# Optimization experiments

Hardware: AMD Instinct MI355X
Metric: run time of the kernel (lower is better)

Reference implementation:

```python
import jax, jax.numpy as jnp
import numpy as np

N_NODES = 100000
N_EDGES = 1600000
IN_FEATS = 128
OUT_FEATS = 128
LN_EPS = 1e-5


def setup_inputs() -> dict:
    key = jax.random.key(0)
    k_h, k_w, k_b, k_src, k_dst = jax.random.split(key, 5)
    stdv = 1.0 / np.sqrt(OUT_FEATS)
    return {
        "h": jax.random.normal(k_h, (N_NODES, IN_FEATS), dtype=jnp.float32),
        "weight": jax.random.uniform(k_w, (IN_FEATS, OUT_FEATS), dtype=jnp.float32, minval=-stdv, maxval=stdv),
        "bias": jax.random.uniform(k_b, (OUT_FEATS,), dtype=jnp.float32, minval=-stdv, maxval=stdv),
        "gamma": jnp.ones((OUT_FEATS,), dtype=jnp.float32),
        "beta": jnp.zeros((OUT_FEATS,), dtype=jnp.float32),
        "src": jax.random.randint(k_src, (N_EDGES,), 0, N_NODES, dtype=jnp.int32),
        "dst": jax.random.randint(k_dst, (N_EDGES,), 0, N_NODES, dtype=jnp.int32),
    }


def reference(h, weight, bias, gamma, beta, src, dst):
    n = h.shape[0]
    # in-degree norm: 1/deg with inf -> 0 (isolated nodes)
    deg = jax.ops.segment_sum(jnp.ones_like(dst, dtype=h.dtype), dst, num_segments=n)
    norm = jnp.where(deg > 0, 1.0 / deg, 0.0)[:, None]  # [N, 1]
    # update_all(copy_src, sum): scatter-add of source features onto destinations
    ah = jax.ops.segment_sum(h[src], dst, num_segments=n)  # [N, in_feats]
    x = ah * norm
    x = x @ weight + bias  # [N, out_feats]
    # LayerNorm over feature dim with affine params
    mu = jnp.mean(x, axis=-1, keepdims=True)
    var = jnp.mean(jnp.square(x - mu), axis=-1, keepdims=True)
    x = (x - mu) * jax.lax.rsqrt(var + LN_EPS) * gamma + beta
    return jax.nn.relu(x)
```

## Files before the change

### kernel.cpp

```cpp
#include <hip/hip_runtime.h>
#include <hip/hip_fp16.h>

#define F 128
#define SCANB 1024
#define NBLK 256
#define GB2 512
#define BSHIFT 7
#define MAXNB 2048
#define SMEM_BYTES 43264

typedef __attribute__((ext_vector_type(8))) short short8;
typedef __attribute__((ext_vector_type(4))) float f32x4;

static __device__ __forceinline__ short f2bf(float f) {
    union { float f; unsigned u; } v; v.f = f;
    unsigned r = v.u + 0x7FFF + ((v.u >> 16) & 1);
    return (short)(r >> 16);
}
static __device__ __forceinline__ __half2 h2(unsigned u) {
    return __builtin_bit_cast(__half2, u);
}
static __device__ __forceinline__ uint4 pack8h(float a0,float a1,float a2,float a3,
                                               float a4,float a5,float a6,float a7) {
    uint4 o;
    o.x = __builtin_bit_cast(unsigned, __floats2half2_rn(a0, a1));
    o.y = __builtin_bit_cast(unsigned, __floats2half2_rn(a2, a3));
    o.z = __builtin_bit_cast(unsigned, __floats2half2_rn(a4, a5));
    o.w = __builtin_bit_cast(unsigned, __floats2half2_rn(a6, a7));
    return o;
}

__global__ __launch_bounds__(256) void k_gemm_hist(
    const float* __restrict__ h, const float* __restrict__ w,
    unsigned* __restrict__ hb, const int* __restrict__ dst,
    int* __restrict__ mat, int* __restrict__ done,
    int n_nodes, int n_edges, int nb, int hblk) {
    __shared__ alignas(16) char smem[SMEM_BYTES];
    const int tid = threadIdx.x;
    const int bid = blockIdx.x;

    if (bid == 0 && tid == 0 && done) *done = 0;

    if (bid < hblk) {
        int* lh = (int*)smem;
        for (int i = tid; i < nb; i += 256) lh[i] = 0;
        __syncthreads();
        const int epb = (n_edges + hblk - 1) / hblk;
        const int e0 = bid * epb, e1 = min(e0 + epb, n_edges);
        for (int e = e0 + tid; e < e1; e += 256)
            atomicAdd(&lh[dst[e] >> BSHIFT], 1);
        __syncthreads();
        for (int i = tid; i < nb; i += 256)
            mat[(size_t)i * NBLK + bid] = lh[i];
        return;
    }

    short* wt = (short*)smem;
    float* xs = (float*)(smem + 34816);
    {
        int n = tid & 127;
        for (int k = tid >> 7; k < 128; k += 2)
            wt[n * 136 + k] = f2bf(w[(size_t)k * 128 + n]);
    }
    __syncthreads();

    const int wv = tid >> 6, l = tid & 63, lr = l & 15, lk = l >> 4, q = l & 15;
    const int step = (gridDim.x - hblk) * 64;
    float* xw = xs + wv * (4 * 132);

    for (int base = (bid - hblk) * 64; base < n_nodes; base += step) {
        const int row = base + wv * 16 + lr;
        const bool valid = row < n_nodes;

        short8 af[4];
        #pragma unroll
        for (int kk = 0; kk < 4; ++kk) {
            int k0 = kk * 32 + lk * 8;
            float4 a0{0,0,0,0}, a1{0,0,0,0};
            if (valid) {
                a0 = *(const float4*)(h + (size_t)row * F + k0);
                a1 = *(const float4*)(h + (size_t)row * F + k0 + 4);
            }
            af[kk] = short8{ f2bf(a0.x), f2bf(a0.y), f2bf(a0.z), f2bf(a0.w),
                             f2bf(a1.x), f2bf(a1.y), f2bf(a1.z), f2bf(a1.w) };
        }
        f32x4 acc[8];
        #pragma unroll
        for (int n = 0; n < 8; ++n) acc[n] = f32x4{0, 0, 0, 0};
        #pragma unroll
        for (int kk = 0; kk < 4; ++kk) {
            const int kb = kk * 32 + lk * 8;
            #pragma unroll
            for (int n = 0; n < 8; ++n) {
                short8 bfr = *(const short8*)(&wt[(n * 16 + lr) * 136 + kb]);
                acc[n] = __builtin_amdgcn_mfma_f32_16x16x32_bf16(af[kk], bfr, acc[n], 0, 0, 0);
            }
        }
        #pragma unroll
        for (int r = 0; r < 4; ++r) {
            #pragma unroll
            for (int n = 0; n < 8; ++n)
                xw[lk * 132 + n * 16 + lr] = acc[n][r];
            int grow = base + wv * 16 + lk * 4 + r;
            float4 a = *(const float4*)&xw[lk * 132 + q * 8];
            float4 b = *(const float4*)&xw[lk * 132 + q * 8 + 4];
            uint4 o = pack8h(a.x, a.y, a.z, a.w, b.x, b.y, b.z, b.w);
            if (grow < n_nodes)
                ((uint4*)hb)[(size_t)grow * 16 + q] = o;
        }
    }
}

__global__ __launch_bounds__(SCANB) void k_scan_ab(const int* in, int* out,
                                                   int* bsum, int* done, int n) {
    __shared__ int tmp[SCANB];
    __shared__ bool amLast;
    int i = blockIdx.x * SCANB + threadIdx.x;
    int v = (i < n) ? in[i] : 0;
    tmp[threadIdx.x] = v;
    __syncthreads();
    for (int off = 1; off < SCANB; off <<= 1) {
        int t = (threadIdx.x >= off) ? tmp[threadIdx.x - off] : 0;
        __syncthreads();
        tmp[threadIdx.x] += t;
        __syncthreads();
    }
    if (i < n) out[i] = tmp[threadIdx.x] - v;
    if (threadIdx.x == SCANB - 1) {
        bsum[blockIdx.x] = tmp[SCANB - 1];
        __threadfence();
        int old = atomicAdd(done, 1);
        amLast = (old == (int)gridDim.x - 1);
    }
    __syncthreads();
    if (amLast) {
        __threadfence();
        const int ns = gridDim.x;
        int w = (threadIdx.x < ns) ? ((volatile int*)bsum)[threadIdx.x] : 0;
        __syncthreads();
        tmp[threadIdx.x] = w;
        __syncthreads();
        for (int off = 1; off < SCANB; off <<= 1) {
            int t = (threadIdx.x >= off) ? tmp[threadIdx.x - off] : 0;
            __syncthreads();
            tmp[threadIdx.x] += t;
            __syncthreads();
        }
        if (threadIdx.x < ns) bsum[threadIdx.x] = tmp[threadIdx.x] - w;
    }
}

__global__ __launch_bounds__(SCANB) void k_scan_a(const int* in, int* out,
                                                  int* bsum, int n) {
    __shared__ int tmp[SCANB];
    int i = blockIdx.x * SCANB + threadIdx.x;
    int v = (i < n) ? in[i] : 0;
    tmp[threadIdx.x] = v;
    __syncthreads();
    for (int off = 1; off < SCANB; off <<= 1) {
        int t = (threadIdx.x >= off) ? tmp[threadIdx.x - off] : 0;
        __syncthreads();
        tmp[threadIdx.x] += t;
        __syncthreads();
    }
    if (i < n) out[i] = tmp[threadIdx.x] - v;
    if (threadIdx.x == SCANB - 1) bsum[blockIdx.x] = tmp[SCANB - 1];
}

__global__ __launch_bounds__(512) void k_scan_b(int* bsum, int nb) {
    __shared__ int tmp[512];
    int i = threadIdx.x;
    int v = (i < nb) ? bsum[i] : 0;
    tmp[i] = v;
    __syncthreads();
    for (int off = 1; off < 512; off <<= 1) {
        int t = (i >= off) ? tmp[i - off] : 0;
        __syncthreads();
        tmp[i] += t;
        __syncthreads();
    }
    if (i < nb) bsum[i] = tmp[i] - v;
}

__global__ __launch_bounds__(SCANB) void k_scan_c(int* out, const int* bsum, int n) {
    int i = blockIdx.x * SCANB + threadIdx.x;
    if (i < n) out[i] += bsum[blockIdx.x];
}

__global__ __launch_bounds__(512) void k_part_scatter(
    const int* __restrict__ src, const int* __restrict__ dst,
    const int* __restrict__ mat, const int* __restrict__ bsum,
    unsigned* __restrict__ binned, int n_edges, int nb, int epb) {
    __shared__ int lbase[MAXNB];
    const int bid = blockIdx.x;
    for (int i = threadIdx.x; i < nb; i += 512) {
        int idx = i * NBLK + bid;
        lbase[i] = mat[idx] + bsum[idx >> 10];
    }
    __syncthreads();
    int e0 = bid * epb;
    int e1 = min(e0 + epb, n_edges);
    for (int e = e0 + threadIdx.x; e < e1; e += 512) {
        int d = dst[e];
        int b = d >> BSHIFT;
        int pos = atomicAdd(&lbase[b], 1);
        binned[pos] = ((unsigned)(d & ((1 << BSHIFT) - 1)) << 25) | (unsigned)src[e];
    }
}

__global__ __launch_bounds__(512) void k_bin_to_csr(
    const unsigned* __restrict__ binned, const int* __restrict__ mat,
    const int* __restrict__ bsum, int* __restrict__ deg, int* __restrict__ offs,
    int* __restrict__ esrc, int n_edges, int n_nodes, int nb) {
    __shared__ int ldeg[128], loffs[128], lcur[128];
    int b = blockIdx.x;
    int i0 = b * NBLK;
    int start = mat[i0] + bsum[i0 >> 10];
    int end = n_edges;
    if (b + 1 < nb) {
        int i1 = (b + 1) * NBLK;
        end = mat[i1] + bsum[i1 >> 10];
    }
    int cnt = end - start;
    int base_node = b << BSHIFT;
    int nn = min(1 << BSHIFT, n_nodes - base_node);
    for (int i = threadIdx.x; i < nn; i += 512) { ldeg[i] = 0; lcur[i] = 0; }
    __syncthreads();
    for (int i = threadIdx.x; i < cnt; i += 512)
        atomicAdd(&ldeg[binned[start + i] >> 25], 1);
    __syncthreads();
    if (threadIdx.x == 0) {
        int run = 0;
        for (int i = 0; i < nn; ++i) { loffs[i] = run; run += ldeg[i]; }
    }
    __syncthreads();
    for (int i = threadIdx.x; i < nn; i += 512) {
        deg[base_node + i]  = ldeg[i];
        offs[base_node + i] = start + loffs[i];
    }
    for (int i = threadIdx.x; i < cnt; i += 512) {
        unsigned p = binned[start + i];
        int ln = p >> 25;
        int pos = start + loffs[ln] + atomicAdd(&lcur[ln], 1);
        esrc[pos] = (int)(p & ((1u << 25) - 1));
    }
}

__global__ __launch_bounds__(256) void k_hist(const int* __restrict__ dst,
                                              int* __restrict__ deg, int n_edges) {
    int e = blockIdx.x * 256 + threadIdx.x;
    if (e < n_edges) atomicAdd(&deg[dst[e]], 1);
}

__global__ __launch_bounds__(256) void k_scatter_idx(
    const int* __restrict__ src, const int* __restrict__ dst,
    const int* __restrict__ offs, int* __restrict__ cursor,
    int* __restrict__ esrc, int n_edges) {
    int e = blockIdx.x * 256 + threadIdx.x;
    if (e >= n_edges) return;
    int d = dst[e];
    int pos = offs[d] + atomicAdd(&cursor[d], 1);
    esrc[pos] = src[e];
}

__global__ __launch_bounds__(256) void k_gather_ln(
    const unsigned* __restrict__ hb, const int* __restrict__ esrc,
    const int* __restrict__ offs, const int* __restrict__ deg,
    const float* __restrict__ bias, const float* __restrict__ gamma,
    const float* __restrict__ beta, float* __restrict__ out, int n_nodes) {
    int t = blockIdx.x * 256 + threadIdx.x;
    int node = t >> 6;
    int l = t & 63;
    if (node >= n_nodes) return;
    const int g = l >> 4;
    const int q = l & 15;

    const int start = offs[node];
    const int dn = deg[node];
    const int end = start + dn;

    __half2 c0 = __floats2half2_rn(0.f, 0.f);
    __half2 c1 = c0, c2 = c0, c3 = c0;
    int i = start;
    for (; i + 16 <= end; i += 16) {
        int s0 = esrc[i + g];
        int s1 = esrc[i + 4 + g];
        int s2 = esrc[i + 8 + g];
        int s3 = esrc[i + 12 + g];
        uint4 v0 = *((const uint4*)(hb + (size_t)s0 * 64 + q * 4));
        uint4 v1 = *((const uint4*)(hb + (size_t)s1 * 64 + q * 4));
        uint4 v2 = *((const uint4*)(hb + (size_t)s2 * 64 + q * 4));
        uint4 v3 = *((const uint4*)(hb + (size_t)s3 * 64 + q * 4));
        c0 = __hadd2(c0, __hadd2(__hadd2(h2(v0.x), h2(v1.x)), __hadd2(h2(v2.x), h2(v3.x))));
        c1 = __hadd2(c1, __hadd2(__hadd2(h2(v0.y), h2(v1.y)), __hadd2(h2(v2.y), h2(v3.y))));
        c2 = __hadd2(c2, __hadd2(__hadd2(h2(v0.z), h2(v1.z)), __hadd2(h2(v2.z), h2(v3.z))));
        c3 = __hadd2(c3, __hadd2(__hadd2(h2(v0.w), h2(v1.w)), __hadd2(h2(v2.w), h2(v3.w))));
    }
    for (; i + 8 <= end; i += 8) {
        int s0 = esrc[i + g];
        int s1 = esrc[i + 4 + g];
        uint4 v0 = *((const uint4*)(hb + (size_t)s0 * 64 + q * 4));
        uint4 v1 = *((const uint4*)(hb + (size_t)s1 * 64 + q * 4));
        c0 = __hadd2(c0, __hadd2(h2(v0.x), h2(v1.x)));
        c1 = __hadd2(c1, __hadd2(h2(v0.y), h2(v1.y)));
        c2 = __hadd2(c2, __hadd2(h2(v0.z), h2(v1.z)));
        c3 = __hadd2(c3, __hadd2(h2(v0.w), h2(v1.w)));
    }
    for (; i < end; i += 4) {
        int e = i + g;
        if (e < end) {
            int s = esrc[e];
            uint4 v = *((const uint4*)(hb + (size_t)s * 64 + q * 4));
            c0 = __hadd2(c0, h2(v.x));
            c1 = __hadd2(c1, h2(v.y));
            c2 = __hadd2(c2, h2(v.z));
            c3 = __hadd2(c3, h2(v.w));
        }
    }
    float2 p0 = __half22float2(c0), p1 = __half22float2(c1);
    float2 p2 = __half22float2(c2), p3 = __half22float2(c3);
    float a0 = p0.x, a1 = p0.y, a2 = p1.x, a3 = p1.y;
    float a4 = p2.x, a5 = p2.y, a6 = p3.x, a7 = p3.y;

    #pragma unroll
    for (int m = 16; m <= 32; m <<= 1) {
        a0 += __shfl_xor(a0, m); a1 += __shfl_xor(a1, m);
        a2 += __shfl_xor(a2, m); a3 += __shfl_xor(a3, m);
        a4 += __shfl_xor(a4, m); a5 += __shfl_xor(a5, m);
        a6 += __shfl_xor(a6, m); a7 += __shfl_xor(a7, m);
    }
    float4 bs0 = *(const float4*)(bias  + q * 8);
    float4 bs1 = *(const float4*)(bias  + q * 8 + 4);
    const float nv = dn > 0 ? 1.0f / (float)dn : 0.0f;
    float f0 = a0 * nv + bs0.x, f1 = a1 * nv + bs0.y;
    float f2 = a2 * nv + bs0.z, f3 = a3 * nv + bs0.w;
    float f4 = a4 * nv + bs1.x, f5 = a5 * nv + bs1.y;
    float f6 = a6 * nv + bs1.z, f7 = a7 * nv + bs1.w;

    float s  = ((f0 + f1) + (f2 + f3)) + ((f4 + f5) + (f6 + f7));
    float q2 = ((f0*f0 + f1*f1) + (f2*f2 + f3*f3)) + ((f4*f4 + f5*f5) + (f6*f6 + f7*f7));
    #pragma unroll
    for (int m = 1; m <= 8; m <<= 1) {
        s  += __shfl_xor(s, m);
        q2 += __shfl_xor(q2, m);
    }
    float mu   = s * (1.0f / F);
    float var  = q2 * (1.0f / F) - mu * mu;
    float rstd = rsqrtf(var + 1e-5f);

    if (g == 0) {
        float4 gm0 = *(const float4*)(gamma + q * 8);
        float4 gm1 = *(const float4*)(gamma + q * 8 + 4);
        float4 bt0 = *(const float4*)(beta  + q * 8);
        float4 bt1 = *(const float4*)(beta  + q * 8 + 4);
        float4 o0, o1;
        o0.x = fmaxf((f0 - mu) * rstd * gm0.x + bt0.x, 0.0f);
        o0.y = fmaxf((f1 - mu) * rstd * gm0.y + bt0.y, 0.0f);
        o0.z = fmaxf((f2 - mu) * rstd * gm0.z + bt0.z, 0.0f);
        o0.w = fmaxf((f3 - mu) * rstd * gm0.w + bt0.w, 0.0f);
        o1.x = fmaxf((f4 - mu) * rstd * gm1.x + bt1.x, 0.0f);
        o1.y = fmaxf((f5 - mu) * rstd * gm1.y + bt1.y, 0.0f);
        o1.z = fmaxf((f6 - mu) * rstd * gm1.z + bt1.z, 0.0f);
        o1.w = fmaxf((f7 - mu) * rstd * gm1.w + bt1.w, 0.0f);
        float* op = out + (size_t)node * F + q * 8;
        *(float4*)op = o0;
        *(float4*)(op + 4) = o1;
    }
}

extern "C" void kernel_launch(void* const* d_in, const int* in_sizes, int n_in,
                              void* d_out, int out_size, void* d_ws, size_t ws_size,
                              hipStream_t stream) {
    const float* h      = (const float*)d_in[0];
    const float* weight = (const float*)d_in[1];
    const float* bias   = (const float*)d_in[2];
    const float* gamma  = (const float*)d_in[3];
    const float* beta   = (const float*)d_in[4];
    const int*   src    = (const int*)d_in[5];
    const int*   dst    = (const int*)d_in[6];

    const int n_nodes = in_sizes[0] / F;
    const int n_edges = in_sizes[5];

    float* x = (float*)d_out;

    const int nb = (n_nodes + (1 << BSHIFT) - 1) >> BSHIFT;
    const int len = nb * NBLK;
    const int nscan = (len + SCANB - 1) / SCANB;
    const bool shift_ok = (nb <= MAXNB) && (nscan <= 512) && (n_nodes <= (1 << 25));

    int* deg    = (int*)d_ws;
    int* offs   = deg + n_nodes;
    int* esrc   = offs + n_nodes;
    unsigned* hb = (unsigned*)(esrc + n_edges);
    int* bsum   = (int*)(hb + (size_t)n_nodes * 64);
    int* done   = bsum + 1023;
    int* mat    = bsum + 1024;
    unsigned* binned = (unsigned*)(mat + (size_t)len);
    int* cursor = mat;

    size_t need_common = ((size_t)2 * n_nodes + (size_t)n_edges + 1024) * sizeof(int)
                       + (size_t)n_nodes * 64 * sizeof(unsigned);
    size_t need_new  = need_common + ((size_t)len + (size_t)n_edges) * sizeof(int);
    size_t need_fall = need_common + (size_t)n_nodes * sizeof(int);
    bool use_new = shift_ok && ws_size >= need_new;

    const int gb = (n_nodes + 63) / 64;

    if (use_new) {
        k_gemm_hist<<<NBLK + GB2, 256, 0, stream>>>(h, weight, hb, dst, mat, done,
                                                    n_nodes, n_edges, nb, NBLK);
        k_scan_ab<<<nscan, SCANB, 0, stream>>>(mat, mat, bsum, done, len);
        const int epb = (n_edges + NBLK - 1) / NBLK;
        k_part_scatter<<<NBLK, 512, 0, stream>>>(src, dst, mat, bsum, binned,
                                                 n_edges, nb, epb);
        k_bin_to_csr<<<nb, 512, 0, stream>>>(binned, mat, bsum, deg, offs, esrc,
                                             n_edges, n_nodes, nb);
        int gblocks = (int)(((size_t)n_nodes * 64 + 255) / 256);
        k_gather_ln<<<gblocks, 256, 0, stream>>>(hb, esrc, offs, deg,
                                                 bias, gamma, beta, x, n_nodes);
    } else if (ws_size >= need_fall) {
        k_gemm_hist<<<gb, 256, 0, stream>>>(h, weight, hb, dst, mat, (int*)nullptr,
                                            n_nodes, n_edges, nb, 0);
        const int nscan2 = (n_nodes + SCANB - 1) / SCANB;
        hipMemsetAsync(deg, 0, (size_t)n_nodes * sizeof(int), stream);
        hipMemsetAsync(cursor, 0, (size_t)n_nodes * sizeof(int), stream);
        k_hist<<<(n_edges + 255) / 256, 256, 0, stream>>>(dst, deg, n_edges);
        k_scan_a<<<nscan2, SCANB, 0, stream>>>(deg, offs, bsum, n_nodes);
        k_scan_b<<<1, 512, 0, stream>>>(bsum, nscan2);
        k_scan_c<<<nscan2, SCANB, 0, stream>>>(offs, bsum, n_nodes);
        k_scatter_idx<<<(n_edges + 255) / 256, 256, 0, stream>>>(
            src, dst, offs, cursor, esrc, n_edges);
        int gblocks = (int)(((size_t)n_nodes * 64 + 255) / 256);
        k_gather_ln<<<gblocks, 256, 0, stream>>>(hb, esrc, offs, deg,
                                                 bias, gamma, beta, x, n_nodes);
    }
}
```

Baseline: 129.0 us.

## Widen CSR bins to 512 nodes and parallelize per-bin offset scan

Enlarges each destination bin from 128 to 512 nodes, which cuts the bin count (and so the count matrix, the scan and the partition bookkeeping) by four. The packed edge word now uses 9 bits for the local node and 23 bits for the source index. The serial single-thread prefix sum inside k_bin_to_csr is replaced by a Hillis-Steele block scan over 512 entries, one per thread. In exchange, each CSR block handles four times as many edges, and the supported node count drops to 2^23. The scan code assumes blockDim equals BS (512).

```diff
diff --git a/kernel.cpp b/kernel.cpp
--- a/kernel.cpp
+++ b/kernel.cpp
@@ -5,7 +5,9 @@
 #define SCANB 1024
 #define NBLK 256
 #define GB2 512
-#define BSHIFT 7
+#define BSHIFT 9
+#define BS (1 << BSHIFT)
+#define PSH 23
 #define MAXNB 2048
 #define SMEM_BYTES 43264
 
@@ -204,7 +206,7 @@
         int d = dst[e];
         int b = d >> BSHIFT;
         int pos = atomicAdd(&lbase[b], 1);
-        binned[pos] = ((unsigned)(d & ((1 << BSHIFT) - 1)) << 25) | (unsigned)src[e];
+        binned[pos] = ((unsigned)(d & (BS - 1)) << PSH) | (unsigned)src[e];
     }
 }
 
@@ -212,7 +214,8 @@
     const unsigned* __restrict__ binned, const int* __restrict__ mat,
     const int* __restrict__ bsum, int* __restrict__ deg, int* __restrict__ offs,
     int* __restrict__ esrc, int n_edges, int n_nodes, int nb) {
-    __shared__ int ldeg[128], loffs[128], lcur[128];
+    __shared__ int ldeg[BS], loffs[BS], lcur[BS];
+    const int tid = threadIdx.x;
     int b = blockIdx.x;
     int i0 = b * NBLK;
     int start = mat[i0] + bsum[i0 >> 10];
@@ -223,26 +226,36 @@
     }
     int cnt = end - start;
     int base_node = b << BSHIFT;
-    int nn = min(1 << BSHIFT, n_nodes - base_node);
-    for (int i = threadIdx.x; i < nn; i += 512) { ldeg[i] = 0; lcur[i] = 0; }
-    __syncthreads();
-    for (int i = threadIdx.x; i < cnt; i += 512)
-        atomicAdd(&ldeg[binned[start + i] >> 25], 1);
-    __syncthreads();
-    if (threadIdx.x == 0) {
-        int run = 0;
-        for (int i = 0; i < nn; ++i) { loffs[i] = run; run += ldeg[i]; }
-    }
-    __syncthreads();
-    for (int i = threadIdx.x; i < nn; i += 512) {
-        deg[base_node + i]  = ldeg[i];
-        offs[base_node + i] = start + loffs[i];
-    }
-    for (int i = threadIdx.x; i < cnt; i += 512) {
+    int nn = min(BS, n_nodes - base_node);
+
+    ldeg[tid] = 0; lcur[tid] = 0;
+    __syncthreads();
+    for (int i = tid; i < cnt; i += 512)
+        atomicAdd(&ldeg[binned[start + i] >> PSH], 1);
+    __syncthreads();
+    int v = ldeg[tid];
+    loffs[tid] = v;
+    __syncthreads();
+    for (int off = 1; off < BS; off <<= 1) {
+        int t = (tid >= off) ? loffs[tid - off] : 0;
+        __syncthreads();
+        loffs[tid] += t;
+        __syncthreads();
+    }
+    int excl = loffs[tid] - v;
+    __syncthreads();
+    loffs[tid] = excl;
+    __syncthreads();
+
+    if (tid < nn) {
+        deg[base_node + tid]  = ldeg[tid];
+        offs[base_node + tid] = start + loffs[tid];
+    }
+    for (int i = tid; i < cnt; i += 512) {
         unsigned p = binned[start + i];
-        int ln = p >> 25;
+        int ln = p >> PSH;
         int pos = start + loffs[ln] + atomicAdd(&lcur[ln], 1);
-        esrc[pos] = (int)(p & ((1u << 25) - 1));
+        esrc[pos] = (int)(p & ((1u << PSH) - 1));
     }
 }
 
@@ -384,10 +397,10 @@
 
     float* x = (float*)d_out;
 
-    const int nb = (n_nodes + (1 << BSHIFT) - 1) >> BSHIFT;
+    const int nb = (n_nodes + BS - 1) >> BSHIFT;
     const int len = nb * NBLK;
     const int nscan = (len + SCANB - 1) / SCANB;
-    const bool shift_ok = (nb <= MAXNB) && (nscan <= 512) && (n_nodes <= (1 << 25));
+    const bool shift_ok = (nb <= MAXNB) && (nscan <= 512) && (n_nodes <= (1 << PSH));
 
     int* deg    = (int*)d_ws;
     int* offs   = deg + n_nodes;
```

New measurement: 123.9 us. 3.9% less time.
